# Performance work log

Hardware: AMD Instinct MI355X
Metric: run time of the kernel (lower is better)

The kernel has to match this reference:

```python
import jax, jax.numpy as jnp
import numpy as np

B, V = 256, 128000
NEG_INF = jnp.float32(-1e30)


def setup_inputs() -> dict:
    key = jax.random.key(0)
    k1, k2, k3 = jax.random.split(key, 3)
    logits = jax.random.normal(k1, (B, V), dtype=jnp.float32) * 2.0
    k = jax.random.randint(k2, (B,), 1, 65)                     # top-k in [1, 64]
    p = 0.5 + 0.5 * jax.random.uniform(k3, (B,), jnp.float32)   # top-p in [0.5, 1.0]
    return {"logits": logits, "k": k, "p": p}


def reference(logits, k, p):
    # softmax over vocab (rbln_top_k_top_p_sample: probs = softmax(logits))
    probs = jax.nn.softmax(logits, axis=-1)                      # [B, V]

    # sort probs descending (torch.ops.rbln.top_k_top_p semantics)
    order = jnp.argsort(-probs, axis=-1)                         # [B, V]
    sp = jnp.take_along_axis(probs, order, axis=-1)              # sorted probs, desc

    ranks = jnp.arange(V)
    topk_mask = ranks[None, :] < k[:, None]                      # keep top-k ranks

    csum = jnp.cumsum(sp, axis=-1)
    # keep tokens whose cumulative mass BEFORE them is < p (always keeps rank 0)
    topp_mask = (csum - sp) < p[:, None]

    keep = topk_mask & topp_mask                                 # [B, V] in sorted space
    filtered = jnp.where(keep, sp, 0.0)
    filtered = filtered / jnp.sum(filtered, axis=-1, keepdims=True)

    # sample from the renormalized filtered distribution (seed=42 as in module)
    logp = jnp.where(keep, jnp.log(jnp.maximum(filtered, 1e-38)), NEG_INF)
    sampled_rank = jax.random.categorical(jax.random.key(42), logp, axis=-1)  # [B]
    sampled = jnp.take_along_axis(order, sampled_rank[:, None], axis=-1)[:, 0]
    return sampled
```

## Files before the change

### kernel.cpp

```cpp
#include <hip/hip_runtime.h>
#include <stdint.h>

#define V 128000
#define V4 (V / 4)
#define BROWS 256
#define CAP 2048
#define NTHREADS 1024
#define T0 16.0f

__device__ __forceinline__ unsigned rotl32(unsigned x, int d) {
  return (x << d) | (x >> (32 - d));
}

__device__ __forceinline__ uint2 threefry2x32(unsigned x0, unsigned x1) {
  const unsigned k0 = 0u, k1 = 42u;
  const unsigned k2 = k0 ^ k1 ^ 0x1BD11BDAu;
  x0 += k0; x1 += k1;
#define TF_RND(r) { x0 += x1; x1 = rotl32(x1, r); x1 ^= x0; }
  TF_RND(13) TF_RND(15) TF_RND(26) TF_RND(6)
  x0 += k1; x1 += k2 + 1u;
  TF_RND(17) TF_RND(29) TF_RND(16) TF_RND(24)
  x0 += k2; x1 += k0 + 2u;
  TF_RND(13) TF_RND(15) TF_RND(26) TF_RND(6)
  x0 += k0; x1 += k1 + 3u;
  TF_RND(17) TF_RND(29) TF_RND(16) TF_RND(24)
  x0 += k1; x1 += k2 + 4u;
  TF_RND(13) TF_RND(15) TF_RND(26) TF_RND(6)
  x0 += k2; x1 += k0 + 5u;
#undef TF_RND
  return make_uint2(x0, x1);
}

__device__ __forceinline__ float gumbel_at(unsigned flat) {
  uint2 r = threefry2x32(0u, flat);
  unsigned bits = r.x ^ r.y;
  float f = __uint_as_float((bits >> 9) | 0x3F800000u) - 1.0f;
  const float TINY = 1.17549435e-38f;
  float u = fmaxf(TINY, f + TINY);
  return -logf(-logf(u));
}

__device__ __forceinline__ unsigned fkey(float v) {
  unsigned u = __float_as_uint(v);
  return (u & 0x80000000u) ? ~u : (u | 0x80000000u);
}
__device__ __forceinline__ float fkey_inv(unsigned u) {
  unsigned r = (u & 0x80000000u) ? (u & 0x7FFFFFFFu) : ~u;
  return __uint_as_float(r);
}

extern "C" __global__ void __launch_bounds__(NTHREADS)
topk_topp_sample_kernel(const float* __restrict__ logits,
                        const int* __restrict__ kin,
                        const float* __restrict__ pin,
                        int* __restrict__ out) {
  const int b = blockIdx.x;
  const int tid = threadIdx.x;

  __shared__ unsigned long long cand[CAP];
  __shared__ unsigned long long topkeys[64];
  __shared__ float zpart[NTHREADS / 64];
  __shared__ float sh_sp[64];
  __shared__ float sh_g[64];
  __shared__ int sh_idx[64];
  __shared__ int cnt;
  __shared__ float shZ;

  const float4* row4 = (const float4*)(logits + (size_t)b * V);
  float T = 6.0f;

  if (tid == 0) cnt = 0;
  __syncthreads();

  const float L2E = 1.44269504088896340736f;
  const float NB  = -16.0f * 1.44269504088896340736f;
  float zs0 = 0.0f, zs1 = 0.0f;

#define PROCV(vv, ii)                                                          \
  {                                                                            \
    float4 v = (vv);                                                           \
    zs0 += __builtin_amdgcn_exp2f(__builtin_fmaf(v.x, L2E, NB));               \
    zs1 += __builtin_amdgcn_exp2f(__builtin_fmaf(v.y, L2E, NB));               \
    zs0 += __builtin_amdgcn_exp2f(__builtin_fmaf(v.z, L2E, NB));               \
    zs1 += __builtin_amdgcn_exp2f(__builtin_fmaf(v.w, L2E, NB));               \
    int base = (ii) * 4;                                                       \
    if (v.x > T) { int pos = atomicAdd(&cnt, 1); if (pos < CAP) cand[pos] = ((unsigned long long)fkey(v.x) << 32) | (unsigned long long)(unsigned)(~(unsigned)(base + 0)); } \
    if (v.y > T) { int pos = atomicAdd(&cnt, 1); if (pos < CAP) cand[pos] = ((unsigned long long)fkey(v.y) << 32) | (unsigned long long)(unsigned)(~(unsigned)(base + 1)); } \
    if (v.z > T) { int pos = atomicAdd(&cnt, 1); if (pos < CAP) cand[pos] = ((unsigned long long)fkey(v.z) << 32) | (unsigned long long)(unsigned)(~(unsigned)(base + 2)); } \
    if (v.w > T) { int pos = atomicAdd(&cnt, 1); if (pos < CAP) cand[pos] = ((unsigned long long)fkey(v.w) << 32) | (unsigned long long)(unsigned)(~(unsigned)(base + 3)); } \
  }

  {
    int i = tid;
    for (; i + NTHREADS < V4; i += 2 * NTHREADS) {
      float4 a = row4[i];
      float4 c = row4[i + NTHREADS];
      PROCV(a, i);
      PROCV(c, i + NTHREADS);
    }
    if (i < V4) {
      float4 a = row4[i];
      PROCV(a, i);
    }
  }
  float s = zs0 + zs1;

#pragma unroll
  for (int off = 32; off > 0; off >>= 1) s += __shfl_down(s, off);
  if ((tid & 63) == 0) zpart[tid >> 6] = s;
  __syncthreads();
  if (tid == 0) {
    float z = 0.0f;
    for (int w = 0; w < NTHREADS / 64; ++w) z += zpart[w];
    shZ = z;
  }
  __syncthreads();

  int attempts = 0;
  while (true) {
    int n = cnt;
    if ((n >= 64 && n <= CAP) || attempts >= 24) break;
    T = (n < 64) ? (T - 2.0f) : (T + 1.0f);
    ++attempts;
    __syncthreads();
    if (tid == 0) cnt = 0;
    __syncthreads();
    for (int i = tid; i < V4; i += NTHREADS) {
      float4 v = row4[i];
      int base = i * 4;
      if (v.x > T) { int pos = atomicAdd(&cnt, 1); if (pos < CAP) cand[pos] = ((unsigned long long)fkey(v.x) << 32) | (unsigned long long)(unsigned)(~(unsigned)(base + 0)); }
      if (v.y > T) { int pos = atomicAdd(&cnt, 1); if (pos < CAP) cand[pos] = ((unsigned long long)fkey(v.y) << 32) | (unsigned long long)(unsigned)(~(unsigned)(base + 1)); }
      if (v.z > T) { int pos = atomicAdd(&cnt, 1); if (pos < CAP) cand[pos] = ((unsigned long long)fkey(v.z) << 32) | (unsigned long long)(unsigned)(~(unsigned)(base + 2)); }
      if (v.w > T) { int pos = atomicAdd(&cnt, 1); if (pos < CAP) cand[pos] = ((unsigned long long)fkey(v.w) << 32) | (unsigned long long)(unsigned)(~(unsigned)(base + 3)); }
    }
    __syncthreads();
  }

  int N = cnt < CAP ? cnt : CAP;

  for (int i = tid; i < N; i += NTHREADS) {
    unsigned long long ki = cand[i];
    int rank = 0;
    for (int j = 0; j < N; ++j) rank += (cand[j] > ki) ? 1 : 0;
    if (rank < 64) topkeys[rank] = ki;
  }
  __syncthreads();

  int M = N < 64 ? N : 64;

  if (tid < M) {
    unsigned long long key = topkeys[tid];
    float v = fkey_inv((unsigned)(key >> 32));
    sh_sp[tid] = expf(v - T0) / shZ;
    sh_idx[tid] = (int)(~((unsigned)(key & 0xFFFFFFFFull)));
    sh_g[tid] = gumbel_at((unsigned)((size_t)b * V + tid));
  }
  __syncthreads();

  if (tid == 0) {
    int kk = kin[b];
    float pp = pin[b];
    float c = 0.0f, S = 0.0f;
    unsigned long long keepmask = 0ull;
    for (int r = 0; r < M; ++r) {
      float sp = sh_sp[r];
      c += sp;
      if (r < kk && (c - sp) < pp) {
        S += sp;
        keepmask |= (1ull << r);
      }
    }
    float best = -1e38f;
    int besti = sh_idx[0];
    for (int r = 0; r < M; ++r) {
      if (!(keepmask & (1ull << r))) continue;
      float lp = logf(fmaxf(sh_sp[r] / S, 1e-38f));
      float y = lp + sh_g[r];
      if (y > best) { best = y; besti = sh_idx[r]; }
    }
    out[b] = besti;
  }
}

extern "C" void kernel_launch(void* const* d_in, const int* in_sizes, int n_in,
                              void* d_out, int out_size, void* d_ws, size_t ws_size,
                              hipStream_t stream) {
  const float* logits = (const float*)d_in[0];
  const int* k = (const int*)d_in[1];
  const float* p = (const float*)d_in[2];
  int* out = (int*)d_out;
  (void)in_sizes; (void)n_in; (void)out_size; (void)d_ws; (void)ws_size;
  topk_topp_sample_kernel<<<BROWS, NTHREADS, 0, stream>>>(logits, k, p, out);
}
```

Before: 202.3 us.

## Split each row across two blocks with a separate merge-and-sample kernel

Each row's streaming pass (softmax denominator plus threshold candidate collection) now runs in two blocks, one per half of the vocabulary, so 512 blocks are launched instead of 256. Each block writes its partial sum and candidates to workspace, and a second 256-thread kernel merges them, re-scans the row only if the count is out of range, ranks the candidates and samples. The streaming loop also skips the per-element threshold checks when the max of each float4 is below the threshold. The aim is better CU occupancy for a bandwidth-bound pass, at the cost of an extra launch, workspace traffic, and an O(N^2) ranking done by fewer threads. The old single-kernel path is kept as a fallback when the workspace is too small.

```diff
diff --git a/kernel.cpp b/kernel.cpp
--- a/kernel.cpp
+++ b/kernel.cpp
@@ -3,10 +3,16 @@
 
 #define V 128000
 #define V4 (V / 4)
+#define HV4 (V4 / 2)
 #define BROWS 256
 #define CAP 2048
+#define CAP_HALF 2048
+#define CAP2 4096
 #define NTHREADS 1024
+#define NT1 1024
+#define NT2 256
 #define T0 16.0f
+#define THR0 6.0f
 
 __device__ __forceinline__ unsigned rotl32(unsigned x, int d) {
   return (x << d) | (x >> (32 - d));
@@ -49,6 +55,185 @@
   return __uint_as_float(r);
 }
 
+extern "C" __global__ void __launch_bounds__(NT1, 8)
+stream_half_kernel(const float* __restrict__ logits,
+                   float* __restrict__ wz,
+                   int* __restrict__ wn,
+                   unsigned long long* __restrict__ wc)
+{
+  const int bid = blockIdx.x;
+  const int b = bid >> 1;
+  const int half = bid & 1;
+  const int tid = threadIdx.x;
+
+  __shared__ unsigned long long cand[CAP_HALF];
+  __shared__ float zpart[NT1 / 64];
+  __shared__ int cnt;
+
+  if (tid == 0) cnt = 0;
+  __syncthreads();
+
+  const float4* row4 = (const float4*)(logits + (size_t)b * V);
+  const float T = THR0;
+  const float L2E = 1.44269504088896340736f;
+  const float NB  = -16.0f * 1.44269504088896340736f;
+  float zs0 = 0.0f, zs1 = 0.0f, zs2 = 0.0f, zs3 = 0.0f;
+
+  const int beg = half * HV4;
+  const int end = beg + HV4;
+
+#define PROCV(vv, ii)                                                          \
+  {                                                                            \
+    float4 v = (vv);                                                           \
+    zs0 += __builtin_amdgcn_exp2f(__builtin_fmaf(v.x, L2E, NB));               \
+    zs1 += __builtin_amdgcn_exp2f(__builtin_fmaf(v.y, L2E, NB));               \
+    zs2 += __builtin_amdgcn_exp2f(__builtin_fmaf(v.z, L2E, NB));               \
+    zs3 += __builtin_amdgcn_exp2f(__builtin_fmaf(v.w, L2E, NB));               \
+    float mx = fmaxf(fmaxf(v.x, v.y), fmaxf(v.z, v.w));                        \
+    if (mx > T) {                                                              \
+      int base = (ii) * 4;                                                     \
+      if (v.x > T) { int pos = atomicAdd(&cnt, 1); if (pos < CAP_HALF) cand[pos] = ((unsigned long long)fkey(v.x) << 32) | (unsigned long long)(unsigned)(~(unsigned)(base + 0)); } \
+      if (v.y > T) { int pos = atomicAdd(&cnt, 1); if (pos < CAP_HALF) cand[pos] = ((unsigned long long)fkey(v.y) << 32) | (unsigned long long)(unsigned)(~(unsigned)(base + 1)); } \
+      if (v.z > T) { int pos = atomicAdd(&cnt, 1); if (pos < CAP_HALF) cand[pos] = ((unsigned long long)fkey(v.z) << 32) | (unsigned long long)(unsigned)(~(unsigned)(base + 2)); } \
+      if (v.w > T) { int pos = atomicAdd(&cnt, 1); if (pos < CAP_HALF) cand[pos] = ((unsigned long long)fkey(v.w) << 32) | (unsigned long long)(unsigned)(~(unsigned)(base + 3)); } \
+    }                                                                          \
+  }
+
+  {
+    int i = beg + tid;
+    for (; i + NT1 < end; i += 2 * NT1) {
+      float4 a = row4[i];
+      float4 c = row4[i + NT1];
+      PROCV(a, i);
+      PROCV(c, i + NT1);
+    }
+    if (i < end) {
+      float4 a = row4[i];
+      PROCV(a, i);
+    }
+  }
+#undef PROCV
+
+  float s = zs0 + zs1 + zs2 + zs3;
+#pragma unroll
+  for (int off = 32; off > 0; off >>= 1) s += __shfl_down(s, off);
+  if ((tid & 63) == 0) zpart[tid >> 6] = s;
+  __syncthreads();
+
+  if (tid == 0) {
+    float z = 0.0f;
+    for (int w = 0; w < NT1 / 64; ++w) z += zpart[w];
+    wz[bid] = z;
+    wn[bid] = cnt;
+  }
+  int m = cnt < CAP_HALF ? cnt : CAP_HALF;
+  for (int j = tid; j < m; j += NT1) wc[(size_t)bid * CAP_HALF + j] = cand[j];
+}
+
+extern "C" __global__ void __launch_bounds__(NT2)
+merge_sample_kernel(const float* __restrict__ logits,
+                    const int* __restrict__ kin,
+                    const float* __restrict__ pin,
+                    const float* __restrict__ wz,
+                    const int* __restrict__ wn,
+                    const unsigned long long* __restrict__ wc,
+                    int* __restrict__ out)
+{
+  const int b = blockIdx.x;
+  const int tid = threadIdx.x;
+
+  __shared__ unsigned long long cand[CAP2];
+  __shared__ unsigned long long topkeys[64];
+  __shared__ float sh_sp[64];
+  __shared__ float sh_g[64];
+  __shared__ int sh_idx[64];
+  __shared__ int cnt;
+
+  const float Z = wz[2 * b] + wz[2 * b + 1];
+  const int n0 = wn[2 * b];
+  const int n1 = wn[2 * b + 1];
+  const bool ok = (n0 <= CAP_HALF) && (n1 <= CAP_HALF);
+
+  int N = 0;
+  if (ok) {
+    for (int j = tid; j < n0; j += NT2)
+      cand[j] = wc[(size_t)(2 * b) * CAP_HALF + j];
+    for (int j = tid; j < n1; j += NT2)
+      cand[n0 + j] = wc[(size_t)(2 * b + 1) * CAP_HALF + j];
+    N = n0 + n1;
+  }
+  __syncthreads();
+
+  int n = ok ? N : (CAP2 + 1);
+  if (!(n >= 64 && n <= CAP2)) {
+    const float4* row4 = (const float4*)(logits + (size_t)b * V);
+    float T = THR0;
+    int attempts = 0;
+    while (!(n >= 64 && n <= CAP2) && attempts < 24) {
+      T = (n < 64) ? (T - 2.0f) : (T + 1.0f);
+      ++attempts;
+      __syncthreads();
+      if (tid == 0) cnt = 0;
+      __syncthreads();
+      for (int i = tid; i < V4; i += NT2) {
+        float4 v = row4[i];
+        int base = i * 4;
+        if (v.x > T) { int pos = atomicAdd(&cnt, 1); if (pos < CAP2) cand[pos] = ((unsigned long long)fkey(v.x) << 32) | (unsigned long long)(unsigned)(~(unsigned)(base + 0)); }
+        if (v.y > T) { int pos = atomicAdd(&cnt, 1); if (pos < CAP2) cand[pos] = ((unsigned long long)fkey(v.y) << 32) | (unsigned long long)(unsigned)(~(unsigned)(base + 1)); }
+        if (v.z > T) { int pos = atomicAdd(&cnt, 1); if (pos < CAP2) cand[pos] = ((unsigned long long)fkey(v.z) << 32) | (unsigned long long)(unsigned)(~(unsigned)(base + 2)); }
+        if (v.w > T) { int pos = atomicAdd(&cnt, 1); if (pos < CAP2) cand[pos] = ((unsigned long long)fkey(v.w) << 32) | (unsigned long long)(unsigned)(~(unsigned)(base + 3)); }
+      }
+      __syncthreads();
+      n = cnt;
+    }
+    N = n < CAP2 ? n : CAP2;
+  }
+  __syncthreads();
+
+  for (int i = tid; i < N; i += NT2) {
+    unsigned long long ki = cand[i];
+    int rank = 0;
+    for (int j = 0; j < N; ++j) rank += (cand[j] > ki) ? 1 : 0;
+    if (rank < 64) topkeys[rank] = ki;
+  }
+  __syncthreads();
+
+  const int M = N < 64 ? N : 64;
+
+  if (tid < M) {
+    unsigned long long key = topkeys[tid];
+    float v = fkey_inv((unsigned)(key >> 32));
+    sh_sp[tid] = expf(v - T0) / Z;
+    sh_idx[tid] = (int)(~((unsigned)(key & 0xFFFFFFFFull)));
+    sh_g[tid] = gumbel_at((unsigned)((size_t)b * V + tid));
+  }
+  __syncthreads();
+
+  if (tid == 0) {
+    int kk = kin[b];
+    float pp = pin[b];
+    float c = 0.0f, S = 0.0f;
+    unsigned long long keepmask = 0ull;
+    for (int r = 0; r < M; ++r) {
+      float sp = sh_sp[r];
+      c += sp;
+      if (r < kk && (c - sp) < pp) {
+        S += sp;
+        keepmask |= (1ull << r);
+      }
+    }
+    float best = -1e38f;
+    int besti = sh_idx[0];
+    for (int r = 0; r < M; ++r) {
+      if (!(keepmask & (1ull << r))) continue;
+      float lp = logf(fmaxf(sh_sp[r] / S, 1e-38f));
+      float y = lp + sh_g[r];
+      if (y > best) { best = y; besti = sh_idx[r]; }
+    }
+    out[b] = besti;
+  }
+}
+
 extern "C" __global__ void __launch_bounds__(NTHREADS)
 topk_topp_sample_kernel(const float* __restrict__ logits,
                         const int* __restrict__ kin,
@@ -67,7 +252,7 @@
   __shared__ float shZ;
 
   const float4* row4 = (const float4*)(logits + (size_t)b * V);
-  float T = 6.0f;
+  float T = THR0;
 
   if (tid == 0) cnt = 0;
   __syncthreads();
@@ -76,7 +261,7 @@
   const float NB  = -16.0f * 1.44269504088896340736f;
   float zs0 = 0.0f, zs1 = 0.0f;
 
-#define PROCV(vv, ii)                                                          \
+#define PROCV1(vv, ii)                                                         \
   {                                                                            \
     float4 v = (vv);                                                           \
     zs0 += __builtin_amdgcn_exp2f(__builtin_fmaf(v.x, L2E, NB));               \
@@ -95,14 +280,15 @@
     for (; i + NTHREADS < V4; i += 2 * NTHREADS) {
       float4 a = row4[i];
       float4 c = row4[i + NTHREADS];
-      PROCV(a, i);
-      PROCV(c, i + NTHREADS);
+      PROCV1(a, i);
+      PROCV1(c, i + NTHREADS);
     }
     if (i < V4) {
       float4 a = row4[i];
-      PROCV(a, i);
-    }
-  }
+      PROCV1(a, i);
+    }
+  }
+#undef PROCV1
   float s = zs0 + zs1;
 
 #pragma unroll
@@ -189,6 +375,16 @@
   const int* k = (const int*)d_in[1];
   const float* p = (const float*)d_in[2];
   int* out = (int*)d_out;
-  (void)in_sizes; (void)n_in; (void)out_size; (void)d_ws; (void)ws_size;
-  topk_topp_sample_kernel<<<BROWS, NTHREADS, 0, stream>>>(logits, k, p, out);
-}
+  (void)in_sizes; (void)n_in; (void)out_size;
+
+  const size_t need = 8192 + (size_t)BROWS * 2 * CAP_HALF * 8;
+  if (d_ws != nullptr && ws_size >= need) {
+    float* wz = (float*)d_ws;
+    int* wn = (int*)((char*)d_ws + 4096);
+    unsigned long long* wc = (unsigned long long*)((char*)d_ws + 8192);
+    stream_half_kernel<<<BROWS * 2, NT1, 0, stream>>>(logits, wz, wn, wc);
+    merge_sample_kernel<<<BROWS, NT2, 0, stream>>>(logits, k, p, wz, wn, wc, out);
+  } else {
+    topk_topp_sample_kernel<<<BROWS, NTHREADS, 0, stream>>>(logits, k, p, out);
+  }
+}
```

Result: slower. 207.8 us (+2.7%).
